# Performance work log

Hardware: AMD Instinct MI355X
Metric: run time of the kernel (lower is better)

The kernel has to match this reference:

```python
import jax, jax.numpy as jnp
import numpy as np
import math

N = 20000      # nodes
E = 640000     # edges (avg degree 32)
G = 128        # g_dim (input features)
H1 = 128       # rgcn output dim
H2 = 128       # transformer output dim
R = 8          # num_relations


def setup_inputs() -> dict:
    key = jax.random.key(0)
    ks = jax.random.split(key, 12)
    x = jax.random.normal(ks[0], (N, G), dtype=jnp.float32)
    edge_index = jax.random.randint(ks[1], (2, E), 0, N)
    edge_type = jax.random.randint(ks[2], (E,), 0, R)
    s_in = 1.0 / math.sqrt(G)
    s_h1 = 1.0 / math.sqrt(H1)
    return {
        'x': x,
        'edge_index': edge_index,
        'edge_type': edge_type,
        # RGCNConv params (per-relation weights + root weight + bias)
        'rgcn_weight': jax.random.normal(ks[3], (R, G, H1), dtype=jnp.float32) * s_in,
        'rgcn_root': jax.random.normal(ks[4], (G, H1), dtype=jnp.float32) * s_in,
        'rgcn_bias': jnp.zeros((H1,), dtype=jnp.float32),
        # TransformerConv params (heads=1): query/key/value + skip linear
        'Wq': jax.random.normal(ks[5], (H1, H2), dtype=jnp.float32) * s_h1,
        'bq': jnp.zeros((H2,), dtype=jnp.float32),
        'Wk': jax.random.normal(ks[6], (H1, H2), dtype=jnp.float32) * s_h1,
        'bk': jnp.zeros((H2,), dtype=jnp.float32),
        'Wv': jax.random.normal(ks[7], (H1, H2), dtype=jnp.float32) * s_h1,
        'bv': jnp.zeros((H2,), dtype=jnp.float32),
        'Ws': jax.random.normal(ks[8], (H1, H2), dtype=jnp.float32) * s_h1,
        'bs': jnp.zeros((H2,), dtype=jnp.float32),
    }


def reference(x, edge_index, edge_type, rgcn_weight, rgcn_root, rgcn_bias,
              Wq, bq, Wk, bk, Wv, bv, Ws, bs):
    n = x.shape[0]
    src, dst = edge_index[0], edge_index[1]

    # ---- RGCNConv (aggr='mean' per relation, root weight + bias) ----
    # transform nodes by every relation, then gather per-edge message
    xr = jnp.einsum('ni,rio->nro', x, rgcn_weight)          # [N, R, H1]
    msg = xr[src, edge_type]                                # [E, H1]
    # per (dst, relation) edge counts for mean aggregation
    cnt = jnp.zeros((n, rgcn_weight.shape[0]), x.dtype).at[dst, edge_type].add(1.0)
    denom = jnp.maximum(cnt[dst, edge_type], 1.0)[:, None]  # [E, 1]
    agg = jnp.zeros((n, rgcn_weight.shape[2]), x.dtype).at[dst].add(msg / denom)
    h = agg + x @ rgcn_root + rgcn_bias
    h = jax.nn.relu(h)

    # ---- TransformerConv (heads=1, concat, root_weight=True) ----
    d = Wq.shape[1]
    q = h @ Wq + bq                                          # [N, H2]
    k = h @ Wk + bk
    v = h @ Wv + bv
    score = jnp.sum(q[dst] * k[src], axis=-1) / math.sqrt(d) # [E]
    # softmax over incoming edges of each destination node
    smax = jax.ops.segment_max(score, dst, num_segments=n)   # [N]
    e = jnp.exp(score - smax[dst])                           # [E]
    den = jax.ops.segment_sum(e, dst, num_segments=n)        # [N]
    alpha = e / jnp.maximum(den[dst], 1e-16)                 # [E]
    out = jax.ops.segment_sum(alpha[:, None] * v[src], dst, num_segments=n)
    out = out + h @ Ws + bs                                  # skip connection
    return jax.nn.relu(out)
```

## Files before the change

kernel.cpp:

```cpp
#include <hip/hip_runtime.h>

typedef unsigned short u16;
typedef unsigned int u32;
typedef __attribute__((ext_vector_type(8))) short short8;
typedef __attribute__((ext_vector_type(4))) float f32x4;

#define NN 20000
#define EE 640000
#define SCAN_BLOCKS 80

__device__ inline u16 f2bf(float f) {
    u32 x = __float_as_uint(f);
    return (u16)((x + 0x7FFFu + ((x >> 16) & 1u)) >> 16);
}
__device__ inline float lo16(u32 w) { return __uint_as_float(w << 16); }
__device__ inline float hi16(u32 w) { return __uint_as_float(w & 0xFFFF0000u); }
__device__ inline u32 packbf(float a, float b) { return ((u32)f2bf(b) << 16) | (u32)f2bf(a); }

#define ZP_N (NN * 8)
#define CX_N (NN * 32)
#define WP_N (128 * 1152 + 4 * 128 * 128 + 512)
__global__ __launch_bounds__(256) void prep_all(const float* __restrict__ x,
                                                const float* rw, const float* root,
                                                const float* Wq, const float* Wk,
                                                const float* Wv, const float* Ws,
                                                const float* bq, const float* bk,
                                                const float* bv, const float* bs,
                                                int* __restrict__ cnt, u16* __restrict__ xb,
                                                u16* wt1, u16* wt2, float* bcat) {
    int idx = blockIdx.x * 256 + threadIdx.x;
    if (idx < ZP_N) {
        cnt[idx] = 0;
        return;
    }
    idx -= ZP_N;
    if (idx < CX_N) {
        float4 v = *(const float4*)(x + (size_t)idx * 4);
        uint2 o;
        o.x = packbf(v.x, v.y);
        o.y = packbf(v.z, v.w);
        *(uint2*)(xb + (size_t)idx * 4) = o;
        return;
    }
    idx -= CX_N;
    const int S1 = 128 * 1152, S2 = 4 * 128 * 128;
    if (idx < S1) {
        int o = idx / 1152, k = idx - o * 1152;
        float v = (k < 1024) ? rw[k * 128 + o] : root[(k - 1024) * 128 + o];
        wt1[idx] = f2bf(v);
    } else if (idx < S1 + S2) {
        int j = idx - S1;
        int y = j >> 14, rem = j & 16383, o = rem >> 7, i = rem & 127;
        const float* W = (y == 0) ? Wq : (y == 1) ? Wk : (y == 2) ? Wv : Ws;
        wt2[j] = f2bf(W[i * 128 + o]);
    } else if (idx < S1 + S2 + 512) {
        int j = idx - (S1 + S2);
        int y = j >> 7, c = j & 127;
        const float* b = (y == 0) ? bq : (y == 1) ? bk : (y == 2) ? bv : bs;
        bcat[j] = b[c];
    }
}

__global__ void count_rank(const int* __restrict__ ei, const int* __restrict__ et,
                           int* __restrict__ cnt, int* __restrict__ rank) {
    int base = blockIdx.x * 1024 + threadIdx.x;
#pragma unroll
    for (int j = 0; j < 4; j++) {
        int e = base + j * 256;
        if (e < EE) {
            int dst = ei[EE + e];
            int r = et[e];
            rank[e] = atomicAdd(&cnt[dst * 8 + r], 1);
        }
    }
}

__global__ __launch_bounds__(256) void scan_phase1(const int* __restrict__ cnt,
                                                   int* __restrict__ deg_pref,
                                                   int* __restrict__ blk_sums) {
    __shared__ int lds[256];
    int t = threadIdx.x;
    int n = blockIdx.x * 256 + t;
    int d = 0;
    if (n < NN) {
        int4 c0 = *(const int4*)(cnt + n * 8);
        int4 c1 = *(const int4*)(cnt + n * 8 + 4);
        d = c0.x + c0.y + c0.z + c0.w + c1.x + c1.y + c1.z + c1.w;
    }
    lds[t] = d;
    __syncthreads();
    for (int o = 1; o < 256; o <<= 1) {
        int v = (t >= o) ? lds[t - o] : 0;
        __syncthreads();
        lds[t] += v;
        __syncthreads();
    }
    if (n < NN) deg_pref[n] = lds[t];
    if (t == 255) blk_sums[blockIdx.x] = lds[255];
}

__global__ void scan_phase2(int* __restrict__ blk_sums) {
    __shared__ int lds[128];
    int t = threadIdx.x;
    int v = (t < SCAN_BLOCKS) ? blk_sums[t] : 0;
    lds[t] = v;
    __syncthreads();
    for (int o = 1; o < 128; o <<= 1) {
        int a = (t >= o) ? lds[t - o] : 0;
        __syncthreads();
        lds[t] += a;
        __syncthreads();
    }
    if (t < SCAN_BLOCKS) blk_sums[t] = lds[t] - v;
}

__global__ __launch_bounds__(256) void scan_phase3(const int* __restrict__ cnt,
                                                   const int* __restrict__ deg_pref,
                                                   const int* __restrict__ blk_sums,
                                                   int* __restrict__ row_off,
                                                   int* __restrict__ srt) {
    int n = blockIdx.x * 256 + threadIdx.x;
    if (n >= NN) return;
    int4 c0 = *(const int4*)(cnt + n * 8);
    int4 c1 = *(const int4*)(cnt + n * 8 + 4);
    int deg = c0.x + c0.y + c0.z + c0.w + c1.x + c1.y + c1.z + c1.w;
    int start = blk_sums[blockIdx.x] + deg_pref[n] - deg;
    row_off[n] = start;
    int sub = start;
    int o[8];
    o[0] = sub; sub += c0.x;
    o[1] = sub; sub += c0.y;
    o[2] = sub; sub += c0.z;
    o[3] = sub; sub += c0.w;
    o[4] = sub; sub += c1.x;
    o[5] = sub; sub += c1.y;
    o[6] = sub; sub += c1.z;
    o[7] = sub; sub += c1.w;
    *(int4*)(srt + n * 8) = make_int4(o[0], o[1], o[2], o[3]);
    *(int4*)(srt + n * 8 + 4) = make_int4(o[4], o[5], o[6], o[7]);
    if (n == NN - 1) row_off[NN] = sub;
}

__global__ void scatter_kernel(const int* __restrict__ ei, const int* __restrict__ et,
                               const int* __restrict__ srt, const int* __restrict__ rank,
                               int* __restrict__ es) {
    int base = blockIdx.x * 1024 + threadIdx.x;
#pragma unroll
    for (int j = 0; j < 4; j++) {
        int e = base + j * 256;
        if (e < EE) {
            int dst = ei[EE + e];
            int src = ei[e];
            int r = et[e];
            es[srt[dst * 8 + r] + rank[e]] = src;
        }
    }
}

__global__ __launch_bounds__(256) void rgcn_agg(const u16* __restrict__ xb,
                                                const int* __restrict__ srt,
                                                const int* __restrict__ cnt,
                                                const int* __restrict__ es,
                                                u16* __restrict__ pre) {
    int gid = blockIdx.x * 16 + (threadIdx.x >> 4);
    int lane = threadIdx.x & 15;
    if (gid >= NN * 9) return;
    int node = gid / 9;
    int slot = gid - node * 9;
    long prebase = (long)node * 1152;
    if (slot == 8) {
        uint4 xv = *(const uint4*)(xb + (long)node * 128 + lane * 8);
        *(uint4*)(pre + prebase + 1024 + lane * 8) = xv;
        return;
    }
    int c = cnt[node * 8 + slot];
    int p0 = srt[node * 8 + slot];
    float inv = 1.0f / (float)(c > 1 ? c : 1);
    float a0 = 0.f, a1 = 0.f, a2 = 0.f, a3 = 0.f, a4 = 0.f, a5 = 0.f, a6 = 0.f, a7 = 0.f;
    int i = 0;
    for (; i + 4 <= c; i += 4) {
        int s0 = es[p0 + i], s1 = es[p0 + i + 1], s2 = es[p0 + i + 2], s3 = es[p0 + i + 3];
        uint4 w0 = *(const uint4*)(xb + (long)s0 * 128 + lane * 8);
        uint4 w1 = *(const uint4*)(xb + (long)s1 * 128 + lane * 8);
        uint4 w2 = *(const uint4*)(xb + (long)s2 * 128 + lane * 8);
        uint4 w3 = *(const uint4*)(xb + (long)s3 * 128 + lane * 8);
        a0 += (lo16(w0.x) + lo16(w1.x)) + (lo16(w2.x) + lo16(w3.x));
        a1 += (hi16(w0.x) + hi16(w1.x)) + (hi16(w2.x) + hi16(w3.x));
        a2 += (lo16(w0.y) + lo16(w1.y)) + (lo16(w2.y) + lo16(w3.y));
        a3 += (hi16(w0.y) + hi16(w1.y)) + (hi16(w2.y) + hi16(w3.y));
        a4 += (lo16(w0.z) + lo16(w1.z)) + (lo16(w2.z) + lo16(w3.z));
        a5 += (hi16(w0.z) + hi16(w1.z)) + (hi16(w2.z) + hi16(w3.z));
        a6 += (lo16(w0.w) + lo16(w1.w)) + (lo16(w2.w) + lo16(w3.w));
        a7 += (hi16(w0.w) + hi16(w1.w)) + (hi16(w2.w) + hi16(w3.w));
    }
    for (; i < c; i++) {
        int s = es[p0 + i];
        uint4 w = *(const uint4*)(xb + (long)s * 128 + lane * 8);
        a0 += lo16(w.x); a1 += hi16(w.x); a2 += lo16(w.y); a3 += hi16(w.y);
        a4 += lo16(w.z); a5 += hi16(w.z); a6 += lo16(w.w); a7 += hi16(w.w);
    }
    uint4 ow;
    ow.x = packbf(a0 * inv, a1 * inv);
    ow.y = packbf(a2 * inv, a3 * inv);
    ow.z = packbf(a4 * inv, a5 * inv);
    ow.w = packbf(a6 * inv, a7 * inv);
    *(uint4*)(pre + prebase + slot * 128 + lane * 8) = ow;
}

__global__ __launch_bounds__(256) void gemm_bm32(const u16* __restrict__ A,
                                                 const u16* __restrict__ Bt,
                                                 const float* __restrict__ bias,
                                                 u16* __restrict__ C, int rows) {
    __shared__ u16 As[32 * 136];
    __shared__ u16 Bs[128 * 136];
    int tid = threadIdx.x;
    int w = tid >> 6;
    int lane = tid & 63;
    int quad = lane >> 4;
    int ml = lane & 15;
    int mt = w & 1;
    int nq = w >> 1;
    int block_m = blockIdx.x * 32;

    f32x4 acc[4];
#pragma unroll
    for (int i = 0; i < 4; i++) acc[i] = (f32x4){0.f, 0.f, 0.f, 0.f};

    int rbase = tid >> 4;
    int cb = (tid & 15) * 8;

    for (int kb = 0; kb < 1152; kb += 128) {
#pragma unroll
        for (int rep = 0; rep < 2; rep++) {
            int r = rbase + rep * 16;
            int gr = block_m + r;
            short8 val = {};
            if (gr < rows) val = *(const short8*)(A + (long)gr * 1152 + kb + cb);
            *(short8*)(As + r * 136 + cb) = val;
        }
#pragma unroll
        for (int rep = 0; rep < 8; rep++) {
            int r = rbase + rep * 16;
            short8 val = *(const short8*)(Bt + (long)r * 1152 + kb + cb);
            *(short8*)(Bs + r * 136 + cb) = val;
        }
        __syncthreads();
#pragma unroll
        for (int ks = 0; ks < 4; ks++) {
            short8 af = *(const short8*)(As + (mt * 16 + ml) * 136 + ks * 32 + quad * 8);
#pragma unroll
            for (int nt = 0; nt < 4; nt++) {
                short8 bfr = *(const short8*)(Bs + (nq * 64 + nt * 16 + ml) * 136 + ks * 32 + quad * 8);
                acc[nt] = __builtin_amdgcn_mfma_f32_16x16x32_bf16(af, bfr, acc[nt], 0, 0, 0);
            }
        }
        __syncthreads();
    }
#pragma unroll
    for (int nt = 0; nt < 4; nt++) {
        int col = nq * 64 + nt * 16 + ml;
        float bv = bias[col];
#pragma unroll
        for (int i = 0; i < 4; i++) {
            int gr = block_m + mt * 16 + quad * 4 + i;
            if (gr < rows) {
                float vv = fmaxf(acc[nt][i] + bv, 0.f);
                C[(long)gr * 128 + col] = f2bf(vv);
            }
        }
    }
}

__global__ __launch_bounds__(256) void gemm_qkvs(const u16* __restrict__ A,
                                                 const u16* __restrict__ Bt,
                                                 const float* __restrict__ bias,
                                                 u16* __restrict__ Cq, u16* __restrict__ Ckv,
                                                 u16* __restrict__ Cs, int rows) {
    int y = blockIdx.y;
    Bt += (long)y * 128 * 128;
    bias += y * 128;
    u16* C;
    int ldc;
    if (y == 0) { C = Cq; ldc = 128; }
    else if (y == 1) { C = Ckv; ldc = 256; }
    else if (y == 2) { C = Ckv + 128; ldc = 256; }
    else { C = Cs; ldc = 128; }

    __shared__ u16 As[64 * 136];
    __shared__ u16 Bs[128 * 136];
    int tid = threadIdx.x;
    int w = tid >> 6;
    int lane = tid & 63;
    int quad = lane >> 4;
    int ml = lane & 15;
    int block_m = blockIdx.x * 64;

    f32x4 acc[8];
#pragma unroll
    for (int i = 0; i < 8; i++) acc[i] = (f32x4){0.f, 0.f, 0.f, 0.f};

    int rbase = tid >> 4;
    int cb = (tid & 15) * 8;

#pragma unroll
    for (int rep = 0; rep < 4; rep++) {
        int r = rbase + rep * 16;
        int gr = block_m + r;
        short8 val = {};
        if (gr < rows) val = *(const short8*)(A + (long)gr * 128 + cb);
        *(short8*)(As + r * 136 + cb) = val;
    }
#pragma unroll
    for (int rep = 0; rep < 8; rep++) {
        int r = rbase + rep * 16;
        short8 val = *(const short8*)(Bt + (long)r * 128 + cb);
        *(short8*)(Bs + r * 136 + cb) = val;
    }
    __syncthreads();
#pragma unroll
    for (int ks = 0; ks < 4; ks++) {
        short8 af = *(const short8*)(As + (w * 16 + ml) * 136 + ks * 32 + quad * 8);
#pragma unroll
        for (int nt = 0; nt < 8; nt++) {
            short8 bfr = *(const short8*)(Bs + (nt * 16 + ml) * 136 + ks * 32 + quad * 8);
            acc[nt] = __builtin_amdgcn_mfma_f32_16x16x32_bf16(af, bfr, acc[nt], 0, 0, 0);
        }
    }
#pragma unroll
    for (int nt = 0; nt < 8; nt++) {
        int col = nt * 16 + ml;
        float bv = bias[col];
#pragma unroll
        for (int i = 0; i < 4; i++) {
            int gr = block_m + w * 16 + quad * 4 + i;
            if (gr < rows) {
                C[(long)gr * ldc + col] = f2bf(acc[nt][i] + bv);
            }
        }
    }
}

__global__ __launch_bounds__(256) void attn_kernel(const u16* __restrict__ q,
                                                   const u16* __restrict__ kv,
                                                   const u16* __restrict__ skip,
                                                   const int* __restrict__ row_off,
                                                   const int* __restrict__ es,
                                                   float* __restrict__ out) {
    int node = blockIdx.x * 16 + (threadIdx.x >> 4);
    int lane = threadIdx.x & 15;
    if (node >= NN) return;
    int p0 = row_off[node], p1 = row_off[node + 1];
    uint4 qw = *(const uint4*)(q + (long)node * 128 + lane * 8);
    float q0 = lo16(qw.x), q1 = hi16(qw.x), q2 = lo16(qw.y), q3 = hi16(qw.y);
    float q4 = lo16(qw.z), q5 = hi16(qw.z), q6 = lo16(qw.w), q7 = hi16(qw.w);
    const float SC = 0.08838834764831845f;
    float l = 0.f;
    float a0 = 0.f, a1 = 0.f, a2 = 0.f, a3 = 0.f, a4 = 0.f, a5 = 0.f, a6 = 0.f, a7 = 0.f;
    int p = p0;
    for (; p + 4 <= p1; p += 4) {
        const u16* b0 = kv + (long)es[p] * 256 + lane * 8;
        const u16* b1 = kv + (long)es[p + 1] * 256 + lane * 8;
        const u16* b2 = kv + (long)es[p + 2] * 256 + lane * 8;
        const u16* b3 = kv + (long)es[p + 3] * 256 + lane * 8;
        uint4 k0 = *(const uint4*)b0;
        uint4 k1 = *(const uint4*)b1;
        uint4 k2 = *(const uint4*)b2;
        uint4 k3 = *(const uint4*)b3;
        uint4 v0 = *(const uint4*)(b0 + 128);
        uint4 v1 = *(const uint4*)(b1 + 128);
        uint4 v2 = *(const uint4*)(b2 + 128);
        uint4 v3 = *(const uint4*)(b3 + 128);
        float t0 = q0 * lo16(k0.x) + q1 * hi16(k0.x) + q2 * lo16(k0.y) + q3 * hi16(k0.y) +
                   q4 * lo16(k0.z) + q5 * hi16(k0.z) + q6 * lo16(k0.w) + q7 * hi16(k0.w);
        float t1 = q0 * lo16(k1.x) + q1 * hi16(k1.x) + q2 * lo16(k1.y) + q3 * hi16(k1.y) +
                   q4 * lo16(k1.z) + q5 * hi16(k1.z) + q6 * lo16(k1.w) + q7 * hi16(k1.w);
        float t2 = q0 * lo16(k2.x) + q1 * hi16(k2.x) + q2 * lo16(k2.y) + q3 * hi16(k2.y) +
                   q4 * lo16(k2.z) + q5 * hi16(k2.z) + q6 * lo16(k2.w) + q7 * hi16(k2.w);
        float t3 = q0 * lo16(k3.x) + q1 * hi16(k3.x) + q2 * lo16(k3.y) + q3 * hi16(k3.y) +
                   q4 * lo16(k3.z) + q5 * hi16(k3.z) + q6 * lo16(k3.w) + q7 * hi16(k3.w);
#pragma unroll
        for (int off = 8; off >= 1; off >>= 1) {
            t0 += __shfl_xor(t0, off, 16);
            t1 += __shfl_xor(t1, off, 16);
            t2 += __shfl_xor(t2, off, 16);
            t3 += __shfl_xor(t3, off, 16);
        }
        float w0 = __expf(fminf(t0 * SC, 70.f));
        float w1 = __expf(fminf(t1 * SC, 70.f));
        float w2 = __expf(fminf(t2 * SC, 70.f));
        float w3 = __expf(fminf(t3 * SC, 70.f));
        l += (w0 + w1) + (w2 + w3);
        a0 += w0 * lo16(v0.x) + w1 * lo16(v1.x) + w2 * lo16(v2.x) + w3 * lo16(v3.x);
        a1 += w0 * hi16(v0.x) + w1 * hi16(v1.x) + w2 * hi16(v2.x) + w3 * hi16(v3.x);
        a2 += w0 * lo16(v0.y) + w1 * lo16(v1.y) + w2 * lo16(v2.y) + w3 * lo16(v3.y);
        a3 += w0 * hi16(v0.y) + w1 * hi16(v1.y) + w2 * hi16(v2.y) + w3 * hi16(v3.y);
        a4 += w0 * lo16(v0.z) + w1 * lo16(v1.z) + w2 * lo16(v2.z) + w3 * lo16(v3.z);
        a5 += w0 * hi16(v0.z) + w1 * hi16(v1.z) + w2 * hi16(v2.z) + w3 * hi16(v3.z);
        a6 += w0 * lo16(v0.w) + w1 * lo16(v1.w) + w2 * lo16(v2.w) + w3 * lo16(v3.w);
        a7 += w0 * hi16(v0.w) + w1 * hi16(v1.w) + w2 * hi16(v2.w) + w3 * hi16(v3.w);
    }
    for (; p < p1; p++) {
        const u16* b = kv + (long)es[p] * 256 + lane * 8;
        uint4 kw = *(const uint4*)b;
        uint4 vw = *(const uint4*)(b + 128);
        float t = q0 * lo16(kw.x) + q1 * hi16(kw.x) + q2 * lo16(kw.y) + q3 * hi16(kw.y) +
                  q4 * lo16(kw.z) + q5 * hi16(kw.z) + q6 * lo16(kw.w) + q7 * hi16(kw.w);
#pragma unroll
        for (int off = 8; off >= 1; off >>= 1) t += __shfl_xor(t, off, 16);
        float w = __expf(fminf(t * SC, 70.f));
        l += w;
        a0 += w * lo16(vw.x);
        a1 += w * hi16(vw.x);
        a2 += w * lo16(vw.y);
        a3 += w * hi16(vw.y);
        a4 += w * lo16(vw.z);
        a5 += w * hi16(vw.z);
        a6 += w * lo16(vw.w);
        a7 += w * hi16(vw.w);
    }
    float invl = (l > 0.f) ? 1.0f / l : 0.f;
    uint4 sw = *(const uint4*)(skip + (long)node * 128 + lane * 8);
    float4 oa, ob;
    oa.x = fmaxf(a0 * invl + lo16(sw.x), 0.f);
    oa.y = fmaxf(a1 * invl + hi16(sw.x), 0.f);
    oa.z = fmaxf(a2 * invl + lo16(sw.y), 0.f);
    oa.w = fmaxf(a3 * invl + hi16(sw.y), 0.f);
    ob.x = fmaxf(a4 * invl + lo16(sw.z), 0.f);
    ob.y = fmaxf(a5 * invl + hi16(sw.z), 0.f);
    ob.z = fmaxf(a6 * invl + lo16(sw.w), 0.f);
    ob.w = fmaxf(a7 * invl + hi16(sw.w), 0.f);
    *(float4*)(out + (long)node * 128 + lane * 8) = oa;
    *(float4*)(out + (long)node * 128 + lane * 8 + 4) = ob;
}

extern "C" void kernel_launch(void* const* d_in, const int* in_sizes, int n_in,
                              void* d_out, int out_size, void* d_ws, size_t ws_size,
                              hipStream_t stream) {
    const float* x = (const float*)d_in[0];
    const int* ei = (const int*)d_in[1];
    const int* et = (const int*)d_in[2];
    const float* rw = (const float*)d_in[3];
    const float* root = (const float*)d_in[4];
    const float* rbias = (const float*)d_in[5];
    const float* Wq = (const float*)d_in[6];
    const float* bq = (const float*)d_in[7];
    const float* Wk = (const float*)d_in[8];
    const float* bk = (const float*)d_in[9];
    const float* Wv = (const float*)d_in[10];
    const float* bv = (const float*)d_in[11];
    const float* Ws = (const float*)d_in[12];
    const float* bs = (const float*)d_in[13];

    char* ws = (char*)d_ws;
    size_t off = 0;
    auto alloc = [&](size_t b) {
        size_t o = off;
        off = (off + b + 255) & ~(size_t)255;
        return o;
    };
    u16* pre = (u16*)(ws + alloc((size_t)NN * 1152 * 2));
    u16* h = (u16*)(ws + alloc((size_t)NN * 128 * 2));
    u16* qv = (u16*)(ws + alloc((size_t)NN * 128 * 2));
    u16* kv = (u16*)(ws + alloc((size_t)NN * 256 * 2));
    u16* skip = (u16*)(ws + alloc((size_t)NN * 128 * 2));
    u16* xb = (u16*)(ws + alloc((size_t)NN * 128 * 2));
    u16* wt1 = (u16*)(ws + alloc((size_t)128 * 1152 * 2));
    u16* wt2 = (u16*)(ws + alloc((size_t)4 * 128 * 128 * 2));
    float* bcat = (float*)(ws + alloc((size_t)512 * 4));
    int* cnt = (int*)(ws + alloc((size_t)NN * 8 * 4));
    int* row_off = (int*)(ws + alloc((size_t)(NN + 1) * 4));
    int* srt = (int*)(ws + alloc((size_t)NN * 8 * 4));
    int* deg_pref = (int*)(ws + alloc((size_t)NN * 4));
    int* blk_sums = (int*)(ws + alloc((size_t)128 * 4));
    int* rank = (int*)(ws + alloc((size_t)EE * 4));
    int* es = (int*)(ws + alloc((size_t)EE * 4));
    (void)ws_size;
    (void)in_sizes;
    (void)n_in;
    (void)out_size;

    prep_all<<<(ZP_N + CX_N + WP_N + 255) / 256, 256, 0, stream>>>(
        x, rw, root, Wq, Wk, Wv, Ws, bq, bk, bv, bs, cnt, xb, wt1, wt2, bcat);

    count_rank<<<(EE + 1023) / 1024, 256, 0, stream>>>(ei, et, cnt, rank);
    scan_phase1<<<SCAN_BLOCKS, 256, 0, stream>>>(cnt, deg_pref, blk_sums);
    scan_phase2<<<1, 128, 0, stream>>>(blk_sums);
    scan_phase3<<<SCAN_BLOCKS, 256, 0, stream>>>(cnt, deg_pref, blk_sums, row_off, srt);
    scatter_kernel<<<(EE + 1023) / 1024, 256, 0, stream>>>(ei, et, srt, rank, es);

    rgcn_agg<<<(NN * 9 + 15) / 16, 256, 0, stream>>>(xb, srt, cnt, es, pre);

    gemm_bm32<<<(NN + 31) / 32, 256, 0, stream>>>(pre, wt1, rbias, h, NN);
    gemm_qkvs<<<dim3((NN + 63) / 64, 4), 256, 0, stream>>>(h, wt2, bcat, qv, kv, skip, NN);

    attn_kernel<<<(NN + 15) / 16, 256, 0, stream>>>(qv, kv, skip, row_off, es, (float*)d_out);
}
```

Baseline: 246.1 us.

## Fuse RGCN mean aggregation into GEMM A-tile staging, drop pre buffer

The per-relation mean aggregation now runs inside the RGCN GEMM: each K-block's A tile (32 nodes x 128 features for one relation or the root slot) is gathered and averaged directly into shared memory instead of being written to and reread from a 46 MB intermediate. This removes one kernel launch and the global round trip of the pre buffer. In exchange, the GEMM blocks now carry irregular gather latency with only 625 blocks and little overlap between gather and MFMA work. The edge count and scatter kernels also process 8 edges per thread instead of 4.

```diff
diff --git a/kernel.cpp b/kernel.cpp
--- a/kernel.cpp
+++ b/kernel.cpp
@@ -63,9 +63,9 @@
 
 __global__ void count_rank(const int* __restrict__ ei, const int* __restrict__ et,
                            int* __restrict__ cnt, int* __restrict__ rank) {
-    int base = blockIdx.x * 1024 + threadIdx.x;
-#pragma unroll
-    for (int j = 0; j < 4; j++) {
+    int base = blockIdx.x * 2048 + threadIdx.x;
+#pragma unroll
+    for (int j = 0; j < 8; j++) {
         int e = base + j * 256;
         if (e < EE) {
             int dst = ei[EE + e];
@@ -144,9 +144,9 @@
 __global__ void scatter_kernel(const int* __restrict__ ei, const int* __restrict__ et,
                                const int* __restrict__ srt, const int* __restrict__ rank,
                                int* __restrict__ es) {
-    int base = blockIdx.x * 1024 + threadIdx.x;
-#pragma unroll
-    for (int j = 0; j < 4; j++) {
+    int base = blockIdx.x * 2048 + threadIdx.x;
+#pragma unroll
+    for (int j = 0; j < 8; j++) {
         int e = base + j * 256;
         if (e < EE) {
             int dst = ei[EE + e];
@@ -157,63 +157,18 @@
     }
 }
 
-__global__ __launch_bounds__(256) void rgcn_agg(const u16* __restrict__ xb,
-                                                const int* __restrict__ srt,
-                                                const int* __restrict__ cnt,
-                                                const int* __restrict__ es,
-                                                u16* __restrict__ pre) {
-    int gid = blockIdx.x * 16 + (threadIdx.x >> 4);
-    int lane = threadIdx.x & 15;
-    if (gid >= NN * 9) return;
-    int node = gid / 9;
-    int slot = gid - node * 9;
-    long prebase = (long)node * 1152;
-    if (slot == 8) {
-        uint4 xv = *(const uint4*)(xb + (long)node * 128 + lane * 8);
-        *(uint4*)(pre + prebase + 1024 + lane * 8) = xv;
-        return;
-    }
-    int c = cnt[node * 8 + slot];
-    int p0 = srt[node * 8 + slot];
-    float inv = 1.0f / (float)(c > 1 ? c : 1);
-    float a0 = 0.f, a1 = 0.f, a2 = 0.f, a3 = 0.f, a4 = 0.f, a5 = 0.f, a6 = 0.f, a7 = 0.f;
-    int i = 0;
-    for (; i + 4 <= c; i += 4) {
-        int s0 = es[p0 + i], s1 = es[p0 + i + 1], s2 = es[p0 + i + 2], s3 = es[p0 + i + 3];
-        uint4 w0 = *(const uint4*)(xb + (long)s0 * 128 + lane * 8);
-        uint4 w1 = *(const uint4*)(xb + (long)s1 * 128 + lane * 8);
-        uint4 w2 = *(const uint4*)(xb + (long)s2 * 128 + lane * 8);
-        uint4 w3 = *(const uint4*)(xb + (long)s3 * 128 + lane * 8);
-        a0 += (lo16(w0.x) + lo16(w1.x)) + (lo16(w2.x) + lo16(w3.x));
-        a1 += (hi16(w0.x) + hi16(w1.x)) + (hi16(w2.x) + hi16(w3.x));
-        a2 += (lo16(w0.y) + lo16(w1.y)) + (lo16(w2.y) + lo16(w3.y));
-        a3 += (hi16(w0.y) + hi16(w1.y)) + (hi16(w2.y) + hi16(w3.y));
-        a4 += (lo16(w0.z) + lo16(w1.z)) + (lo16(w2.z) + lo16(w3.z));
-        a5 += (hi16(w0.z) + hi16(w1.z)) + (hi16(w2.z) + hi16(w3.z));
-        a6 += (lo16(w0.w) + lo16(w1.w)) + (lo16(w2.w) + lo16(w3.w));
-        a7 += (hi16(w0.w) + hi16(w1.w)) + (hi16(w2.w) + hi16(w3.w));
-    }
-    for (; i < c; i++) {
-        int s = es[p0 + i];
-        uint4 w = *(const uint4*)(xb + (long)s * 128 + lane * 8);
-        a0 += lo16(w.x); a1 += hi16(w.x); a2 += lo16(w.y); a3 += hi16(w.y);
-        a4 += lo16(w.z); a5 += hi16(w.z); a6 += lo16(w.w); a7 += hi16(w.w);
-    }
-    uint4 ow;
-    ow.x = packbf(a0 * inv, a1 * inv);
-    ow.y = packbf(a2 * inv, a3 * inv);
-    ow.z = packbf(a4 * inv, a5 * inv);
-    ow.w = packbf(a6 * inv, a7 * inv);
-    *(uint4*)(pre + prebase + slot * 128 + lane * 8) = ow;
-}
-
-__global__ __launch_bounds__(256) void gemm_bm32(const u16* __restrict__ A,
+__global__ __launch_bounds__(256) void rgcn_gemm(const u16* __restrict__ xb,
+                                                 const int* __restrict__ srt,
+                                                 const int* __restrict__ cnt,
+                                                 const int* __restrict__ es,
                                                  const u16* __restrict__ Bt,
                                                  const float* __restrict__ bias,
                                                  u16* __restrict__ C, int rows) {
     __shared__ u16 As[32 * 136];
     __shared__ u16 Bs[128 * 136];
     int tid = threadIdx.x;
+    int g = tid >> 4;
+    int lane16 = tid & 15;
     int w = tid >> 6;
     int lane = tid & 63;
     int quad = lane >> 4;
@@ -229,20 +184,58 @@
     int rbase = tid >> 4;
     int cb = (tid & 15) * 8;
 
-    for (int kb = 0; kb < 1152; kb += 128) {
-#pragma unroll
-        for (int rep = 0; rep < 2; rep++) {
-            int r = rbase + rep * 16;
-            int gr = block_m + r;
-            short8 val = {};
-            if (gr < rows) val = *(const short8*)(A + (long)gr * 1152 + kb + cb);
-            *(short8*)(As + r * 136 + cb) = val;
-        }
+#pragma unroll 1
+    for (int kb = 0; kb < 9; kb++) {
 #pragma unroll
         for (int rep = 0; rep < 8; rep++) {
             int r = rbase + rep * 16;
-            short8 val = *(const short8*)(Bt + (long)r * 1152 + kb + cb);
+            short8 val = *(const short8*)(Bt + (long)r * 1152 + kb * 128 + cb);
             *(short8*)(Bs + r * 136 + cb) = val;
+        }
+#pragma unroll
+        for (int rep = 0; rep < 2; rep++) {
+            int nl = g + rep * 16;
+            int node = block_m + nl;
+            uint4 ow = {0u, 0u, 0u, 0u};
+            if (node < rows) {
+                if (kb == 8) {
+                    ow = *(const uint4*)(xb + (long)node * 128 + lane16 * 8);
+                } else {
+                    int c = cnt[node * 8 + kb];
+                    int p0 = srt[node * 8 + kb];
+                    float inv = 1.0f / (float)(c > 1 ? c : 1);
+                    float a0 = 0.f, a1 = 0.f, a2 = 0.f, a3 = 0.f,
+                          a4 = 0.f, a5 = 0.f, a6 = 0.f, a7 = 0.f;
+                    int i = 0;
+                    for (; i + 4 <= c; i += 4) {
+                        int s0 = es[p0 + i], s1 = es[p0 + i + 1],
+                            s2 = es[p0 + i + 2], s3 = es[p0 + i + 3];
+                        uint4 w0 = *(const uint4*)(xb + (long)s0 * 128 + lane16 * 8);
+                        uint4 w1 = *(const uint4*)(xb + (long)s1 * 128 + lane16 * 8);
+                        uint4 w2 = *(const uint4*)(xb + (long)s2 * 128 + lane16 * 8);
+                        uint4 w3 = *(const uint4*)(xb + (long)s3 * 128 + lane16 * 8);
+                        a0 += (lo16(w0.x) + lo16(w1.x)) + (lo16(w2.x) + lo16(w3.x));
+                        a1 += (hi16(w0.x) + hi16(w1.x)) + (hi16(w2.x) + hi16(w3.x));
+                        a2 += (lo16(w0.y) + lo16(w1.y)) + (lo16(w2.y) + lo16(w3.y));
+                        a3 += (hi16(w0.y) + hi16(w1.y)) + (hi16(w2.y) + hi16(w3.y));
+                        a4 += (lo16(w0.z) + lo16(w1.z)) + (lo16(w2.z) + lo16(w3.z));
+                        a5 += (hi16(w0.z) + hi16(w1.z)) + (hi16(w2.z) + hi16(w3.z));
+                        a6 += (lo16(w0.w) + lo16(w1.w)) + (lo16(w2.w) + lo16(w3.w));
+                        a7 += (hi16(w0.w) + hi16(w1.w)) + (hi16(w2.w) + hi16(w3.w));
+                    }
+                    for (; i < c; i++) {
+                        int s = es[p0 + i];
+                        uint4 wv = *(const uint4*)(xb + (long)s * 128 + lane16 * 8);
+                        a0 += lo16(wv.x); a1 += hi16(wv.x); a2 += lo16(wv.y); a3 += hi16(wv.y);
+                        a4 += lo16(wv.z); a5 += hi16(wv.z); a6 += lo16(wv.w); a7 += hi16(wv.w);
+                    }
+                    ow.x = packbf(a0 * inv, a1 * inv);
+                    ow.y = packbf(a2 * inv, a3 * inv);
+                    ow.z = packbf(a4 * inv, a5 * inv);
+                    ow.w = packbf(a6 * inv, a7 * inv);
+                }
+            }
+            *(uint4*)(As + nl * 136 + lane16 * 8) = ow;
         }
         __syncthreads();
 #pragma unroll
@@ -458,7 +451,6 @@
         off = (off + b + 255) & ~(size_t)255;
         return o;
     };
-    u16* pre = (u16*)(ws + alloc((size_t)NN * 1152 * 2));
     u16* h = (u16*)(ws + alloc((size_t)NN * 128 * 2));
     u16* qv = (u16*)(ws + alloc((size_t)NN * 128 * 2));
     u16* kv = (u16*)(ws + alloc((size_t)NN * 256 * 2));
@@ -482,15 +474,13 @@
     prep_all<<<(ZP_N + CX_N + WP_N + 255) / 256, 256, 0, stream>>>(
         x, rw, root, Wq, Wk, Wv, Ws, bq, bk, bv, bs, cnt, xb, wt1, wt2, bcat);
 
-    count_rank<<<(EE + 1023) / 1024, 256, 0, stream>>>(ei, et, cnt, rank);
+    count_rank<<<(EE + 2047) / 2048, 256, 0, stream>>>(ei, et, cnt, rank);
     scan_phase1<<<SCAN_BLOCKS, 256, 0, stream>>>(cnt, deg_pref, blk_sums);
     scan_phase2<<<1, 128, 0, stream>>>(blk_sums);
     scan_phase3<<<SCAN_BLOCKS, 256, 0, stream>>>(cnt, deg_pref, blk_sums, row_off, srt);
-    scatter_kernel<<<(EE + 1023) / 1024, 256, 0, stream>>>(ei, et, srt, rank, es);
-
-    rgcn_agg<<<(NN * 9 + 15) / 16, 256, 0, stream>>>(xb, srt, cnt, es, pre);
-
-    gemm_bm32<<<(NN + 31) / 32, 256, 0, stream>>>(pre, wt1, rbias, h, NN);
+    scatter_kernel<<<(EE + 2047) / 2048, 256, 0, stream>>>(ei, et, srt, rank, es);
+
+    rgcn_gemm<<<(NN + 31) / 32, 256, 0, stream>>>(xb, srt, cnt, es, wt1, rbias, h, NN);
     gemm_qkvs<<<dim3((NN + 63) / 64, 4), 256, 0, stream>>>(h, wt2, bcat, qv, kv, skip, NN);
 
     attn_kernel<<<(NN + 15) / 16, 256, 0, stream>>>(qv, kv, skip, row_off, es, (float*)d_out);
```

After: 262.0 us. +6.5%, slower.
